# Performance work log

Measured on AMD Instinct MI355X. Metric: run time of the kernel, lower is better.

## Reference

```python
import math
import jax, jax.numpy as jnp
import numpy as np

NUM_HEADS = 16
HEAD_DIM = 64
NB_FEATURES = 256
EPS = 1e-06
DATA_NORM = HEAD_DIM ** (-0.25)


def setup_inputs() -> dict:
    key = jax.random.key(0)
    ks = jax.random.split(key, 5)
    B, N, C = 4, 4096, 1024
    x = jax.random.normal(ks[0], (B, N, C), dtype=jnp.float32)
    w_qkv = jax.random.normal(ks[1], (C, 3 * C), dtype=jnp.float32) * (C ** -0.5)
    b_qkv = jnp.zeros((3 * C,), dtype=jnp.float32)
    w_out = jax.random.normal(ks[2], (C, C), dtype=jnp.float32) * (C ** -0.5)
    b_out = jnp.zeros((C,), dtype=jnp.float32)
    proj = jax.random.normal(ks[3], (NUM_HEADS, NB_FEATURES, HEAD_DIM), dtype=jnp.float32)
    proj = proj / jnp.linalg.norm(proj, axis=-1, keepdims=True)  # F.normalize(dim=-1)
    return {"x": x, "w_qkv": w_qkv, "b_qkv": b_qkv, "w_out": w_out, "b_out": b_out,
            "proj_matrix": proj}


def _feature_map(x, proj):
    # x: [b,h,n,d], proj: [h,m,d] -> [b,h,n,m]
    x = x * DATA_NORM
    x_proj = jnp.einsum('bhnd,hmd->bhnm', x, proj)
    sq_norms = 0.5 * jnp.sum(x * x, axis=-1, keepdims=True)
    x_proj = x_proj - sq_norms
    x_proj = x_proj - jnp.max(x_proj, axis=-1, keepdims=True)
    return (jnp.exp(x_proj) + EPS) / math.sqrt(NB_FEATURES)


def reference(x, w_qkv, b_qkv, w_out, b_out, proj_matrix):
    B, N, C = x.shape
    h, d = NUM_HEADS, HEAD_DIM
    qkv = x @ w_qkv + b_qkv                     # [B,N,3C]
    q, k, v = jnp.split(qkv, 3, axis=-1)
    to_heads = lambda z: z.reshape(B, N, h, d).transpose(0, 2, 1, 3)  # [B,h,N,d]
    q, k, v = to_heads(q), to_heads(k), to_heads(v)

    q_prime = _feature_map(q, proj_matrix)      # [B,h,N,m]
    k_prime = _feature_map(k, proj_matrix)      # [B,h,N,m]

    k_sum = jnp.sum(k_prime, axis=2)                          # [B,h,m]
    kv = jnp.einsum('bhnm,bhnd->bhmd', k_prime, v)            # [B,h,m,d]
    numerator = jnp.einsum('bhnm,bhmd->bhnd', q_prime, kv)    # [B,h,N,d]
    denominator = jnp.einsum('bhnm,bhm->bhn', q_prime, k_sum) + EPS
    out = numerator / denominator[..., None]

    out = out.transpose(0, 2, 1, 3).reshape(B, N, C)
    return out @ w_out + b_out
```

## Files before the change

kernel.cpp:

```cpp
#include <hip/hip_runtime.h>
#include <hip/hip_bf16.h>
#include <stdint.h>


#define DN 0.35355339059327379f
#define EPSF 1e-6f
#define INV_SQRT_M 0.0625f

typedef __attribute__((ext_vector_type(8))) short bf16x8;
typedef __attribute__((ext_vector_type(4))) float f32x4;

static __device__ __forceinline__ short f2bf(float f) {
    __hip_bfloat16 h = __float2bfloat16(f);
    return *(short*)&h;
}
static __device__ __forceinline__ void gload16(const void* g, void* l) {
    __builtin_amdgcn_global_load_lds(
        (const __attribute__((address_space(1))) void*)g,
        (__attribute__((address_space(3))) void*)l,
        16, 0, 0);
}

__global__ __launch_bounds__(256) void conv_x(const float* __restrict__ X,
                                              short* __restrict__ Xb) {
    int i = blockIdx.x * 256 + threadIdx.x;
    float4 v = ((const float4*)X)[i];
    short4 o;
    o.x = f2bf(v.x); o.y = f2bf(v.y); o.z = f2bf(v.z); o.w = f2bf(v.w);
    ((short4*)Xb)[i] = o;
}

__global__ __launch_bounds__(256) void convt_w(const float* __restrict__ W,
                                               short* __restrict__ WT,
                                               int K, int NN) {
    __shared__ short tile[64][66];
    int t = threadIdx.x;
    int k0 = blockIdx.y * 64, n0 = blockIdx.x * 64;
    for (int i = t; i < 4096; i += 256) {
        int r = i >> 6, c = i & 63;
        tile[r][c] = f2bf(W[(size_t)(k0 + r) * NN + n0 + c]);
    }
    __syncthreads();
    for (int i = t; i < 4096; i += 256) {
        int r = i >> 6, c = i & 63;
        WT[(size_t)(n0 + r) * K + k0 + c] = tile[c][r];
    }
}

__global__ __launch_bounds__(256) void conv_proj(const float* __restrict__ proj,
                                                 short* __restrict__ pjb) {
    int e = blockIdx.x * 256 + threadIdx.x;
    int m = (e >> 6) & 255, d = e & 63;
    int base = e & ~63;
    pjb[base + (d ^ ((m & 7) << 3))] = f2bf(proj[e]);
}

__device__ __forceinline__ void gemm_core128(const short* __restrict__ A,
                                             const short* __restrict__ BT,
                                             int rowBase, int colBase,
                                             char* smem, f32x4 acc[4][4]) {
    const int K = 1024;
    int t = threadIdx.x, lane = t & 63, w = t >> 6;
    int li = lane & 15, g = lane >> 4;
    int wm = w >> 1, wn = w & 1;

    const char* aSrc[4]; const char* bSrc[4]; int aOff[4];
#pragma unroll
    for (int c = 0; c < 4; ++c) {
        int idx = c * 256 + t;
        int r = idx >> 3, s = t & 7;
        aOff[c] = idx * 16;
        aSrc[c] = (const char*)(A + (size_t)(rowBase + r) * K + ((s ^ (r & 7)) * 8));
        bSrc[c] = (const char*)(BT + (size_t)(colBase + r) * K + ((s ^ (r & 7)) * 8));
    }
#pragma unroll
    for (int m = 0; m < 4; ++m)
#pragma unroll
        for (int n = 0; n < 4; ++n) acc[m][n] = (f32x4){0.f, 0.f, 0.f, 0.f};

#pragma unroll
    for (int c = 0; c < 4; ++c) {
        gload16(aSrc[c], smem + aOff[c]);
        gload16(bSrc[c], smem + 16384 + aOff[c]);
    }

    int swz = (li & 7) << 4;

    for (int tt = 0; tt < 16; ++tt) {
        int cur = tt & 1;
        if (tt < 15) {
            char* d = smem + (cur ^ 1) * 32768;
#pragma unroll
            for (int c = 0; c < 4; ++c) {
                gload16(aSrc[c] + (size_t)(tt + 1) * 128, d + aOff[c]);
                gload16(bSrc[c] + (size_t)(tt + 1) * 128, d + 16384 + aOff[c]);
            }
            asm volatile("s_waitcnt vmcnt(8)" ::: "memory");
        } else {
            asm volatile("s_waitcnt vmcnt(0)" ::: "memory");
        }
        __builtin_amdgcn_sched_barrier(0);
        __builtin_amdgcn_s_barrier();
        __builtin_amdgcn_sched_barrier(0);
        __builtin_amdgcn_s_setprio(1);
        const char* bA = smem + cur * 32768;
        const char* bB = bA + 16384;
#pragma unroll
        for (int ks = 0; ks < 2; ++ks) {
            int kb = ks * 64 + g * 16;
            bf16x8 af[4], bv[4];
#pragma unroll
            for (int m = 0; m < 4; ++m)
                af[m] = *(const bf16x8*)(bA + (wm * 64 + m * 16 + li) * 128 + (kb ^ swz));
#pragma unroll
            for (int n = 0; n < 4; ++n)
                bv[n] = *(const bf16x8*)(bB + (wn * 64 + n * 16 + li) * 128 + (kb ^ swz));
#pragma unroll
            for (int m = 0; m < 4; ++m)
#pragma unroll
                for (int n = 0; n < 4; ++n)
                    acc[m][n] = __builtin_amdgcn_mfma_f32_16x16x32_bf16(
                        af[m], bv[n], acc[m][n], 0, 0, 0);
        }
        __builtin_amdgcn_s_setprio(0);
        __builtin_amdgcn_sched_barrier(0);
        __builtin_amdgcn_s_barrier();
        __builtin_amdgcn_sched_barrier(0);
    }
}

__global__ __launch_bounds__(256, 2) void mfma_gemm_qkv(
        const short* __restrict__ A, const short* __restrict__ BT,
        const float* __restrict__ bias,
        short* __restrict__ Qh, short* __restrict__ Kh, short* __restrict__ Vt) {
    __shared__ __align__(16) char smem[65536];
    int t = threadIdx.x, lane = t & 63, w = t >> 6;
    int li = lane & 15, g = lane >> 4, wm = w >> 1, wn = w & 1;
    int lin = blockIdx.x;
    int bx = lin % 24, by = lin / 24;
    int rowBase = by * 128, colBase = bx * 128;

    f32x4 acc[4][4];
    gemm_core128(A, BT, rowBase, colBase, smem, acc);

    float bcol[4];
#pragma unroll
    for (int n = 0; n < 4; ++n) bcol[n] = bias[colBase + wn * 64 + n * 16 + li];
    int whichB = colBase >> 10;

    if (whichB == 2) {
#pragma unroll
        for (int n = 0; n < 4; ++n) {
            int gc = colBase + wn * 64 + n * 16 + li;
            int hh = (gc & 1023) >> 6, dd = gc & 63;
#pragma unroll
            for (int m = 0; m < 4; ++m) {
                int gr0 = rowBase + wm * 64 + m * 16 + g * 4;
                int b = gr0 >> 12, nn0 = gr0 & 4095;
                short4 o;
                o.x = f2bf(acc[m][n][0] + bcol[n]);
                o.y = f2bf(acc[m][n][1] + bcol[n]);
                o.z = f2bf(acc[m][n][2] + bcol[n]);
                o.w = f2bf(acc[m][n][3] + bcol[n]);
                int nsw = (nn0 & ~63) | ((nn0 & 63) ^ ((dd & 7) << 3));
                *(short4*)&Vt[((size_t)(b * 16 + hh) * 64 + dd) * 4096 + nsw] = o;
            }
        }
    } else {
        short* dst = (whichB == 0) ? Qh : Kh;
        int hh = ((colBase + wn * 64) & 1023) >> 6;
        float* wreg = (float*)(smem + w * 8704);
#pragma unroll
        for (int r = 0; r < 2; ++r) {
#pragma unroll
            for (int mi = 0; mi < 2; ++mi)
#pragma unroll
                for (int n = 0; n < 4; ++n)
#pragma unroll
                    for (int jj = 0; jj < 4; ++jj)
                        wreg[(mi * 16 + g * 4 + jj) * 68 + n * 16 + li] =
                            (acc[2 * r + mi][n][jj] + bcol[n]) * DN;
            int row = lane >> 1, h2 = lane & 1;
            int tok = rowBase + wm * 64 + r * 32 + row;
            int b = tok >> 12, nn = tok & 4095;
            size_t base = ((size_t)(b * 16 + hh) * 4096 + nn) * 64;
#pragma unroll
            for (int k = 0; k < 4; ++k) {
                float4 v0 = *(const float4*)&wreg[row * 68 + h2 * 32 + k * 8];
                float4 v1 = *(const float4*)&wreg[row * 68 + h2 * 32 + k * 8 + 4];
                bf16x8 ov;
                ov[0] = f2bf(v0.x); ov[1] = f2bf(v0.y);
                ov[2] = f2bf(v0.z); ov[3] = f2bf(v0.w);
                ov[4] = f2bf(v1.x); ov[5] = f2bf(v1.y);
                ov[6] = f2bf(v1.z); ov[7] = f2bf(v1.w);
                int dgrp = (h2 * 4 + k) ^ (tok & 7);
                *(bf16x8*)&dst[base + dgrp * 8] = ov;
            }
        }
    }
}

__global__ __launch_bounds__(256, 2) void mfma_gemm_out(
        const short* __restrict__ A, const short* __restrict__ BT,
        const float* __restrict__ bias, float* __restrict__ C) {
    __shared__ __align__(16) char smem[65536];
    int t = threadIdx.x, lane = t & 63, w = t >> 6;
    int li = lane & 15, g = lane >> 4, wm = w >> 1, wn = w & 1;
    int lin = blockIdx.x;
    int bx = lin & 7, by = lin >> 3;
    int rowBase = by * 128, colBase = bx * 128;

    f32x4 acc[4][4];
    gemm_core128(A, BT, rowBase, colBase, smem, acc);

    float bcol[4];
#pragma unroll
    for (int n = 0; n < 4; ++n) bcol[n] = bias[colBase + wn * 64 + n * 16 + li];
    float* wreg = (float*)(smem + w * 8704);
#pragma unroll
    for (int r = 0; r < 2; ++r) {
#pragma unroll
        for (int mi = 0; mi < 2; ++mi)
#pragma unroll
            for (int n = 0; n < 4; ++n)
#pragma unroll
                for (int jj = 0; jj < 4; ++jj)
                    wreg[(mi * 16 + g * 4 + jj) * 68 + n * 16 + li] =
                        acc[2 * r + mi][n][jj] + bcol[n];
        int row = lane >> 1, h2 = lane & 1;
        int gr = rowBase + wm * 64 + r * 32 + row;
        float* cp = C + (size_t)gr * 1024 + colBase + wn * 64 + h2 * 32;
#pragma unroll
        for (int k = 0; k < 8; ++k)
            *(float4*)&cp[k * 4] = *(const float4*)&wreg[row * 68 + h2 * 32 + k * 4];
    }
}

__global__ __launch_bounds__(256) void fmap_mfma(const short* __restrict__ Kh,
                                                 const short* __restrict__ Vt,
                                                 const short* __restrict__ pjb,
                                                 float* __restrict__ kvpart,
                                                 float* __restrict__ kspart) {
    int bh = blockIdx.y, ch = blockIdx.x, h = bh & 15;
    int t = threadIdx.x, lane = t & 63, w = t >> 6;
    int g = lane >> 4, li = lane & 15;
    __shared__ __align__(16) short pj[256 * 64];
    __shared__ __align__(16) short kt[64 * 64];
    __shared__ __align__(16) short vt[64 * 64];
    __shared__ __align__(16) short Pl[4][64 * 40];
    __shared__ __align__(16) float maxw[4][64];

    const short* kbase = Kh + ((size_t)bh * 4096 + ch * 512) * 64;
    const short* vbase = Vt + (size_t)bh * 64 * 4096 + ch * 512;

    {
        const short* psrc = pjb + (size_t)h * 16384;
#pragma unroll
        for (int c2 = 0; c2 < 8; ++c2) {
            int c = 8 * w + c2;
            gload16(psrc + c * 512 + lane * 8, pj + c * 512);
        }
#pragma unroll
        for (int c2 = 0; c2 < 2; ++c2) {
            int c = 2 * w + c2;
            gload16(kbase + c * 512 + lane * 8, kt + c * 512);
            int d = 8 * c + (lane >> 3);
            gload16(vbase + (size_t)d * 4096 + (lane & 7) * 8, vt + c * 512);
        }
    }
    __syncthreads();

    f32x4 acc[4][4];
#pragma unroll
    for (int i = 0; i < 4; ++i)
#pragma unroll
        for (int j = 0; j < 4; ++j) acc[i][j] = (f32x4){0.f, 0.f, 0.f, 0.f};
    float ksacc[4] = {0.f, 0.f, 0.f, 0.f};

    int swz = (li & 7) << 4;

    for (int tile = 0; tile < 8; ++tile) {
        bf16x8 rk0, rk1, rv0, rv1;
        if (tile < 7) {
            int c0 = 2 * w, c1 = 2 * w + 1;
            size_t kof = (size_t)((tile + 1) * 64) * 64;
            rk0 = *(const bf16x8*)(kbase + kof + c0 * 512 + lane * 8);
            rk1 = *(const bf16x8*)(kbase + kof + c1 * 512 + lane * 8);
            int d0 = 8 * c0 + (lane >> 3), d1 = 8 * c1 + (lane >> 3);
            rv0 = *(const bf16x8*)(vbase + (size_t)d0 * 4096 + (tile + 1) * 64 + (lane & 7) * 8);
            rv1 = *(const bf16x8*)(vbase + (size_t)d1 * 4096 + (tile + 1) * 64 + (lane & 7) * 8);
        }

        f32x4 sacc[4][4];
#pragma unroll
        for (int i = 0; i < 4; ++i)
#pragma unroll
            for (int j = 0; j < 4; ++j) sacc[i][j] = (f32x4){0.f, 0.f, 0.f, 0.f};
#pragma unroll
        for (int ks = 0; ks < 2; ++ks) {
            int kb = ks * 64 + g * 16;
            bf16x8 afr[4], bfr[4];
#pragma unroll
            for (int ni = 0; ni < 4; ++ni)
                afr[ni] = *(const bf16x8*)((const char*)kt +
                           (16 * ni + li) * 128 + (kb ^ swz));
#pragma unroll
            for (int mi = 0; mi < 4; ++mi)
                bfr[mi] = *(const bf16x8*)((const char*)pj +
                           (64 * w + 16 * mi + li) * 128 + (kb ^ swz));
#pragma unroll
            for (int ni = 0; ni < 4; ++ni)
#pragma unroll
                for (int mi = 0; mi < 4; ++mi)
                    sacc[ni][mi] = __builtin_amdgcn_mfma_f32_16x16x32_bf16(
                        afr[ni], bfr[mi], sacc[ni][mi], 0, 0, 0);
        }

        float mxl[4][4];
#pragma unroll
        for (int ni = 0; ni < 4; ++ni)
#pragma unroll
            for (int jj = 0; jj < 4; ++jj) {
                float m0 = fmaxf(sacc[ni][0][jj], sacc[ni][1][jj]);
                float m1 = fmaxf(sacc[ni][2][jj], sacc[ni][3][jj]);
                mxl[ni][jj] = fmaxf(m0, m1);
            }
#pragma unroll
        for (int off = 1; off <= 8; off <<= 1)
#pragma unroll
            for (int ni = 0; ni < 4; ++ni)
#pragma unroll
                for (int jj = 0; jj < 4; ++jj)
                    mxl[ni][jj] = fmaxf(mxl[ni][jj], __shfl_xor(mxl[ni][jj], off));
        if (li == 0) {
#pragma unroll
            for (int ni = 0; ni < 4; ++ni)
                *(float4*)&maxw[w][16 * ni + 4 * g] =
                    make_float4(mxl[ni][0], mxl[ni][1], mxl[ni][2], mxl[ni][3]);
        }
        __syncthreads();

#pragma unroll
        for (int hf = 0; hf < 2; ++hf) {
#pragma unroll
            for (int ni2 = 0; ni2 < 2; ++ni2) {
                int ni = 2 * hf + ni2;
                float4 a0 = *(const float4*)&maxw[0][16 * ni + 4 * g];
                float4 a1 = *(const float4*)&maxw[1][16 * ni + 4 * g];
                float4 a2 = *(const float4*)&maxw[2][16 * ni + 4 * g];
                float4 a3 = *(const float4*)&maxw[3][16 * ni + 4 * g];
                float mm[4];
                mm[0] = fmaxf(fmaxf(a0.x, a1.x), fmaxf(a2.x, a3.x));
                mm[1] = fmaxf(fmaxf(a0.y, a1.y), fmaxf(a2.y, a3.y));
                mm[2] = fmaxf(fmaxf(a0.z, a1.z), fmaxf(a2.z, a3.z));
                mm[3] = fmaxf(fmaxf(a0.w, a1.w), fmaxf(a2.w, a3.w));
#pragma unroll
                for (int mi = 0; mi < 4; ++mi) {
                    float p0 = (__expf(sacc[ni][mi][0] - mm[0]) + EPSF) * INV_SQRT_M;
                    float p1 = (__expf(sacc[ni][mi][1] - mm[1]) + EPSF) * INV_SQRT_M;
                    float p2 = (__expf(sacc[ni][mi][2] - mm[2]) + EPSF) * INV_SQRT_M;
                    float p3 = (__expf(sacc[ni][mi][3] - mm[3]) + EPSF) * INV_SQRT_M;
                    ksacc[mi] += (p0 + p1) + (p2 + p3);
                    uint32_t u0 = (uint32_t)(uint16_t)f2bf(p0) |
                                  ((uint32_t)(uint16_t)f2bf(p1) << 16);
                    uint32_t u1 = (uint32_t)(uint16_t)f2bf(p2) |
                                  ((uint32_t)(uint16_t)f2bf(p3) << 16);
                    int m_l = 16 * mi + li;
                    *(uint2*)((char*)Pl[w] + m_l * 80 + 32 * ni2 + 8 * g) =
                        make_uint2(u0, u1);
                }
            }
#pragma unroll
            for (int mi = 0; mi < 4; ++mi) {
                bf16x8 pa = *(const bf16x8*)((const char*)Pl[w] +
                             (16 * mi + li) * 80 + 16 * g);
#pragma unroll
                for (int di = 0; di < 4; ++di) {
                    bf16x8 bv = *(const bf16x8*)((const char*)vt +
                                 (16 * di + li) * 128 + ((64 * hf + 16 * g) ^ swz));
                    acc[mi][di] = __builtin_amdgcn_mfma_f32_16x16x32_bf16(
                        pa, bv, acc[mi][di], 0, 0, 0);
                }
            }
        }
        __syncthreads();
        if (tile < 7) {
            int c0 = 2 * w, c1 = 2 * w + 1;
            *(bf16x8*)((char*)kt + c0 * 1024 + lane * 16) = rk0;
            *(bf16x8*)((char*)kt + c1 * 1024 + lane * 16) = rk1;
            *(bf16x8*)((char*)vt + c0 * 1024 + lane * 16) = rv0;
            *(bf16x8*)((char*)vt + c1 * 1024 + lane * 16) = rv1;
            __syncthreads();
        }
    }

#pragma unroll
    for (int mi = 0; mi < 4; ++mi) {
        ksacc[mi] += __shfl_xor(ksacc[mi], 16);
        ksacc[mi] += __shfl_xor(ksacc[mi], 32);
    }
    if (lane < 16) {
#pragma unroll
        for (int mi = 0; mi < 4; ++mi)
            kspart[(bh * 8 + ch) * 256 + 64 * w + 16 * mi + li] = ksacc[mi];
    }
    float* kvb = kvpart + (size_t)(bh * 8 + ch) * 16384;
#pragma unroll
    for (int mi = 0; mi < 4; ++mi)
#pragma unroll
        for (int di = 0; di < 4; ++di) {
            int d = 16 * di + li, m0 = 64 * w + 16 * mi + 4 * g;
            *(float4*)&kvb[d * 256 + m0] =
                make_float4(acc[mi][di][0], acc[mi][di][1],
                            acc[mi][di][2], acc[mi][di][3]);
        }
}

__global__ __launch_bounds__(256) void reduce_kv(const float* __restrict__ kvpart,
                                                 const float* __restrict__ kspart,
                                                 short* __restrict__ kvsT) {
    int bh = blockIdx.y, bx = blockIdx.x, t = threadIdx.x;
    if (bx < 4) {
#pragma unroll
        for (int i = 0; i < 16; ++i) {
            int idx = t + i * 256;
            int d = 16 * bx + (idx >> 8), m = idx & 255;
            float s = 0.f;
            size_t base = ((size_t)(bh * 8) * 64 + d) * 256 + m;
#pragma unroll
            for (int c = 0; c < 8; ++c) s += kvpart[base + (size_t)c * 16384];
            int widx = (m & 128) + ((m & 127) ^ ((d & 7) << 3));
            kvsT[((size_t)bh * 80 + d) * 256 + widx] = f2bf(s);
        }
    } else {
        float s = 0.f;
#pragma unroll
        for (int c = 0; c < 8; ++c) s += kspart[((bh * 8 + c) << 8) + t];
        kvsT[((size_t)bh * 80 + 64) * 256 + t] = f2bf(s);
        for (int i = t; i < 15 * 256; i += 256) {
            int r = 65 + (i >> 8), cc = i & 255;
            kvsT[((size_t)bh * 80 + r) * 256 + cc] = 0;
        }
    }
}

__global__ __launch_bounds__(256) void contract_mfma(
        const short* __restrict__ Qh,
        const short* __restrict__ pjb,
        const short* __restrict__ kvsT,
        short* __restrict__ attn) {
    int bh = blockIdx.y, rb = blockIdx.x, h = bh & 15, b = bh >> 4;
    int t = threadIdx.x, lane = t & 63, w = t >> 6;
    __shared__ __align__(16) short qs[128 * 64];
    __shared__ __align__(16) short pj[128 * 64];
    __shared__ __align__(16) short Pl[64 * 128];
    __shared__ __align__(16) short kvl[80 * 128];

    {
        const short* src = Qh + ((size_t)bh * 4096 + rb * 128) * 64;
#pragma unroll
        for (int c2 = 0; c2 < 4; ++c2) {
            int c = 4 * w + c2;
            gload16(src + (c * 8 + (lane >> 3)) * 64 + (lane & 7) * 8,
                    qs + c * 512);
        }
    }

    f32x4 acc5[2][5];
#pragma unroll
    for (int rg = 0; rg < 2; ++rg)
#pragma unroll
        for (int i = 0; i < 5; ++i) acc5[rg][i] = (f32x4){0.f, 0.f, 0.f, 0.f};

    int g = lane >> 4, li = lane & 15;

    for (int half = 0; half < 2; ++half) {
        const short* psrc = pjb + (size_t)h * 16384 + half * 8192;
#pragma unroll
        for (int c2 = 0; c2 < 4; ++c2) {
            int c = 4 * w + c2;
            gload16(psrc + (c * 8 + (lane >> 3)) * 64 + (lane & 7) * 8,
                    pj + c * 512);
        }
        const short* ksrc = kvsT + (size_t)bh * 80 * 256 + half * 128;
#pragma unroll
        for (int c2 = 0; c2 < 5; ++c2) {
            int c = 5 * w + c2;
            gload16(ksrc + (c * 4 + (lane >> 4)) * 256 + (lane & 15) * 8,
                    kvl + c * 512);
        }
        __syncthreads();

#pragma unroll
        for (int rg = 0; rg < 2; ++rg) {
            f32x4 sacc[2][4];
#pragma unroll
            for (int mi = 0; mi < 2; ++mi)
#pragma unroll
                for (int ni = 0; ni < 4; ++ni) sacc[mi][ni] = (f32x4){0.f, 0.f, 0.f, 0.f};
#pragma unroll
            for (int ks = 0; ks < 2; ++ks) {
                int kbyte = ks * 64 + g * 16;
                bf16x8 afr[2], bfr[4];
#pragma unroll
                for (int mi = 0; mi < 2; ++mi) {
                    int mr = 32 * w + 16 * mi + li;
                    afr[mi] = *(const bf16x8*)((const char*)pj +
                               mr * 128 + (kbyte ^ ((mr & 7) << 4)));
                }
#pragma unroll
                for (int ni = 0; ni < 4; ++ni) {
                    int qr = rg * 64 + 16 * ni + li;
                    bfr[ni] = *(const bf16x8*)((const char*)qs +
                               qr * 128 + (kbyte ^ ((qr & 7) << 4)));
                }
#pragma unroll
                for (int mi = 0; mi < 2; ++mi)
#pragma unroll
                    for (int ni = 0; ni < 4; ++ni)
                        sacc[mi][ni] = __builtin_amdgcn_mfma_f32_16x16x32_bf16(
                            afr[mi], bfr[ni], sacc[mi][ni], 0, 0, 0);
            }

#pragma unroll
            for (int mi = 0; mi < 2; ++mi) {
                int m0 = 32 * w + 16 * mi + 4 * g;
#pragma unroll
                for (int ni = 0; ni < 4; ++ni) {
                    int row = 16 * ni + li;
                    float e0 = (__expf(sacc[mi][ni][0]) + EPSF) * INV_SQRT_M;
                    float e1 = (__expf(sacc[mi][ni][1]) + EPSF) * INV_SQRT_M;
                    float e2 = (__expf(sacc[mi][ni][2]) + EPSF) * INV_SQRT_M;
                    float e3 = (__expf(sacc[mi][ni][3]) + EPSF) * INV_SQRT_M;
                    uint32_t u0 = (uint32_t)(uint16_t)f2bf(e0) |
                                  ((uint32_t)(uint16_t)f2bf(e1) << 16);
                    uint32_t u1 = (uint32_t)(uint16_t)f2bf(e2) |
                                  ((uint32_t)(uint16_t)f2bf(e3) << 16);
                    int byte = row * 256 + ((m0 * 2) ^ ((row & 7) << 4));
                    *(uint2*)((char*)Pl + byte) = make_uint2(u0, u1);
                }
            }
            __syncthreads();

            int rowA = 16 * w + li;
            int abase = rowA * 256;
            int asw = (rowA & 7) << 4;
#pragma unroll
            for (int ks = 0; ks < 4; ++ks) {
                int kbyte = ks * 64 + g * 16;
                bf16x8 pa = *(const bf16x8*)((const char*)Pl + abase + (kbyte ^ asw));
#pragma unroll
                for (int ni = 0; ni < 5; ++ni) {
                    int rowB = 16 * ni + li;
                    bf16x8 bv = *(const bf16x8*)((const char*)kvl +
                                 rowB * 256 + (kbyte ^ ((rowB & 7) << 4)));
                    acc5[rg][ni] = __builtin_amdgcn_mfma_f32_16x16x32_bf16(
                        pa, bv, acc5[rg][ni], 0, 0, 0);
                }
            }
            __syncthreads();
        }
    }

#pragma unroll
    for (int rg = 0; rg < 2; ++rg) {
        float dj[4];
#pragma unroll
        for (int jj = 0; jj < 4; ++jj)
            dj[jj] = __shfl(acc5[rg][4][jj], lane & 48) + EPSF;
#pragma unroll
        for (int ni = 0; ni < 4; ++ni) {
            int d = 16 * ni + li;
#pragma unroll
            for (int jj = 0; jj < 4; ++jj) {
                int n = rb * 128 + rg * 64 + 16 * w + 4 * g + jj;
                attn[((size_t)b * 4096 + n) * 1024 + h * 64 + d] =
                    f2bf(acc5[rg][ni][jj] / dj[jj]);
            }
        }
    }
}

extern "C" void kernel_launch(void* const* d_in, const int* in_sizes, int n_in,
                              void* d_out, int out_size, void* d_ws, size_t ws_size,
                              hipStream_t stream) {
    const float* x      = (const float*)d_in[0];
    const float* w_qkv  = (const float*)d_in[1];
    const float* b_qkv  = (const float*)d_in[2];
    const float* w_out  = (const float*)d_in[3];
    const float* b_out  = (const float*)d_in[4];
    const float* proj   = (const float*)d_in[5];
    float* out = (float*)d_out;

    char* w = (char*)d_ws;
    short* xb     = (short*)(w);
    short* wqT    = (short*)(w + 33554432);
    short* wOT    = (short*)(w + 39845888);
    short* Qh     = (short*)(w + 41943040);
    short* Kh     = (short*)(w + 75497472);
    short* Vt     = (short*)(w + 109051904);
    float* kvpart = (float*)(w);
    float* kspart = (float*)(w + 142606336);
    short* kvsT   = (short*)(w + 143130624);
    short* pjb    = (short*)(w + 145752064);
    short* attn   = Kh;

    conv_x<<<dim3(16384), 256, 0, stream>>>(x, xb);
    convt_w<<<dim3(48, 16), 256, 0, stream>>>(w_qkv, wqT, 1024, 3072);
    convt_w<<<dim3(16, 16), 256, 0, stream>>>(w_out, wOT, 1024, 1024);
    conv_proj<<<dim3(1024), 256, 0, stream>>>(proj, pjb);
    mfma_gemm_qkv<<<dim3(3072), 256, 0, stream>>>(xb, wqT, b_qkv, Qh, Kh, Vt);
    fmap_mfma<<<dim3(8, 64), 256, 0, stream>>>(Kh, Vt, pjb, kvpart, kspart);
    reduce_kv<<<dim3(5, 64), 256, 0, stream>>>(kvpart, kspart, kvsT);
    contract_mfma<<<dim3(32, 64), 256, 0, stream>>>(Qh, pjb, kvsT, attn);
    mfma_gemm_out<<<dim3(1024), 256, 0, stream>>>(attn, wOT, b_out, out);
}
```

Measured before the change: 321.7 us.

## Use 256x256 GEMM tiles with 8 waves and 4-phase quadrant pipelining

Replaces the 128x128, 4-wave GEMM core with a 256x256 tile computed by 8 waves in 512-thread blocks, using 128KB of LDS. Each K-step is split into four quadrant phases that interleave staged global-to-LDS loads with MFMA work under fine-grained vmcnt waits. The larger tile halves global/L2 traffic per FLOP for both the QKV and output projections. The cost is a single block per CU, a much more complex schedule, and fewer blocks: 256 for the output GEMM, which may underfill the GPU.

```diff
diff --git a/kernel.cpp b/kernel.cpp
--- a/kernel.cpp
+++ b/kernel.cpp
@@ -55,185 +55,241 @@
     pjb[base + (d ^ ((m & 7) << 3))] = f2bf(proj[e]);
 }
 
-__device__ __forceinline__ void gemm_core128(const short* __restrict__ A,
-                                             const short* __restrict__ BT,
-                                             int rowBase, int colBase,
-                                             char* smem, f32x4 acc[4][4]) {
+template<int Q, int S>
+static __device__ __forceinline__ void phase_compute(
+        const char* smem, int tt, int wm, int wn, int li, int g, int swz,
+        f32x4 (&acc)[2][4][2][2]) {
+    const char* bA = smem + ((tt & 1) << 16) + (Q << 14);
+    const char* bB = smem + ((tt & 1) << 16) + 32768 + (S << 14);
+    bf16x8 af[4][2], bf[2][2];
+#pragma unroll
+    for (int fr = 0; fr < 4; ++fr) {
+        int row = wm * 64 + fr * 16 + li;
+#pragma unroll
+        for (int kk = 0; kk < 2; ++kk)
+            af[fr][kk] = *(const bf16x8*)(bA + row * 128 + ((kk * 64 + g * 16) ^ swz));
+    }
+#pragma unroll
+    for (int fn = 0; fn < 2; ++fn) {
+        int row = wn * 32 + fn * 16 + li;
+#pragma unroll
+        for (int kk = 0; kk < 2; ++kk)
+            bf[fn][kk] = *(const bf16x8*)(bB + row * 128 + ((kk * 64 + g * 16) ^ swz));
+    }
+    __builtin_amdgcn_s_setprio(1);
+#pragma unroll
+    for (int kk = 0; kk < 2; ++kk)
+#pragma unroll
+        for (int fr = 0; fr < 4; ++fr)
+#pragma unroll
+            for (int fn = 0; fn < 2; ++fn)
+                acc[Q][fr][S][fn] = __builtin_amdgcn_mfma_f32_16x16x32_bf16(
+                    af[fr][kk], bf[fn][kk], acc[Q][fr][S][fn], 0, 0, 0);
+    __builtin_amdgcn_s_setprio(0);
+}
+
+static __device__ __forceinline__ void gemm_core256(const short* __restrict__ A,
+                                                    const short* __restrict__ BT,
+                                                    int rowBase, int colBase,
+                                                    char* smem,
+                                                    f32x4 (&acc)[2][4][2][2]) {
     const int K = 1024;
-    int t = threadIdx.x, lane = t & 63, w = t >> 6;
+    int t = threadIdx.x, lane = t & 63;
     int li = lane & 15, g = lane >> 4;
-    int wm = w >> 1, wn = w & 1;
-
-    const char* aSrc[4]; const char* bSrc[4]; int aOff[4];
-#pragma unroll
-    for (int c = 0; c < 4; ++c) {
-        int idx = c * 256 + t;
-        int r = idx >> 3, s = t & 7;
-        aOff[c] = idx * 16;
-        aSrc[c] = (const char*)(A + (size_t)(rowBase + r) * K + ((s ^ (r & 7)) * 8));
-        bSrc[c] = (const char*)(BT + (size_t)(colBase + r) * K + ((s ^ (r & 7)) * 8));
-    }
-#pragma unroll
-    for (int m = 0; m < 4; ++m)
-#pragma unroll
-        for (int n = 0; n < 4; ++n) acc[m][n] = (f32x4){0.f, 0.f, 0.f, 0.f};
-
-#pragma unroll
-    for (int c = 0; c < 4; ++c) {
-        gload16(aSrc[c], smem + aOff[c]);
-        gload16(bSrc[c], smem + 16384 + aOff[c]);
-    }
-
+    int w = t >> 6, wm = w >> 2, wn = w & 3;
     int swz = (li & 7) << 4;
 
-    for (int tt = 0; tt < 16; ++tt) {
-        int cur = tt & 1;
-        if (tt < 15) {
-            char* d = smem + (cur ^ 1) * 32768;
-#pragma unroll
-            for (int c = 0; c < 4; ++c) {
-                gload16(aSrc[c] + (size_t)(tt + 1) * 128, d + aOff[c]);
-                gload16(bSrc[c] + (size_t)(tt + 1) * 128, d + 16384 + aOff[c]);
-            }
-            asm volatile("s_waitcnt vmcnt(8)" ::: "memory");
-        } else {
-            asm volatile("s_waitcnt vmcnt(0)" ::: "memory");
-        }
-        __builtin_amdgcn_sched_barrier(0);
-        __builtin_amdgcn_s_barrier();
-        __builtin_amdgcn_sched_barrier(0);
-        __builtin_amdgcn_s_setprio(1);
-        const char* bA = smem + cur * 32768;
-        const char* bB = bA + 16384;
-#pragma unroll
-        for (int ks = 0; ks < 2; ++ks) {
-            int kb = ks * 64 + g * 16;
-            bf16x8 af[4], bv[4];
-#pragma unroll
-            for (int m = 0; m < 4; ++m)
-                af[m] = *(const bf16x8*)(bA + (wm * 64 + m * 16 + li) * 128 + (kb ^ swz));
-#pragma unroll
-            for (int n = 0; n < 4; ++n)
-                bv[n] = *(const bf16x8*)(bB + (wn * 64 + n * 16 + li) * 128 + (kb ^ swz));
-#pragma unroll
-            for (int m = 0; m < 4; ++m)
-#pragma unroll
-                for (int n = 0; n < 4; ++n)
-                    acc[m][n] = __builtin_amdgcn_mfma_f32_16x16x32_bf16(
-                        af[m], bv[n], acc[m][n], 0, 0, 0);
-        }
-        __builtin_amdgcn_s_setprio(0);
-        __builtin_amdgcn_sched_barrier(0);
-        __builtin_amdgcn_s_barrier();
-        __builtin_amdgcn_sched_barrier(0);
-    }
-}
-
-__global__ __launch_bounds__(256, 2) void mfma_gemm_qkv(
+    int idxA = t, idxB = 512 + t;
+    int rA = idxA >> 3, sA = idxA & 7;
+    int rB = idxB >> 3, sB = idxB & 7;
+    const char* Ab = (const char*)(A + (size_t)rowBase * K);
+    const char* Bb = (const char*)(BT + (size_t)colBase * K);
+    int srcOffA = rA * 2048 + ((sA ^ (rA & 7)) * 16);
+    int srcOffB = rB * 2048 + ((sB ^ (rB & 7)) * 16);
+    int dstOffA = idxA * 16, dstOffB = idxB * 16;
+
+#define STG(op_, half_, tile_) do {                                           \
+    char* d_ = smem + (((tile_) & 1) << 16) + ((op_) << 15) + ((half_) << 14);\
+    const char* s_ = ((op_) ? Bb : Ab) + (half_) * 262144 + (tile_) * 128;    \
+    gload16(s_ + srcOffA, d_ + dstOffA);                                      \
+    gload16(s_ + srcOffB, d_ + dstOffB);                                      \
+} while (0)
+
+#define PH(q_, s_, vm_, dost_, sop_, shalf_, stile_) do {                     \
+    if (dost_) STG(sop_, shalf_, stile_);                                     \
+    asm volatile("s_waitcnt vmcnt(" #vm_ ")" ::: "memory");                   \
+    __builtin_amdgcn_sched_barrier(0);                                        \
+    __builtin_amdgcn_s_barrier();                                             \
+    __builtin_amdgcn_sched_barrier(0);                                        \
+    phase_compute<q_, s_>(smem, tt, wm, wn, li, g, swz, acc);                 \
+} while (0)
+
+#pragma unroll
+    for (int q = 0; q < 2; ++q)
+#pragma unroll
+        for (int fr = 0; fr < 4; ++fr)
+#pragma unroll
+            for (int s = 0; s < 2; ++s)
+#pragma unroll
+                for (int fn = 0; fn < 2; ++fn)
+                    acc[q][fr][s][fn] = (f32x4){0.f, 0.f, 0.f, 0.f};
+
+    STG(1, 0, 0);
+    STG(0, 1, 0);
+    STG(0, 0, 0);
+    STG(1, 1, 0);
+    STG(1, 0, 1);
+    STG(0, 1, 1);
+
+    for (int tt = 0; tt < 14; ++tt) {
+        PH(0, 0,  8, true, 0, 0, tt + 1);
+        PH(1, 0, 12, true, 1, 1, tt + 1);
+        PH(1, 1, 10, true, 1, 0, tt + 2);
+        PH(0, 1, 12, true, 0, 1, tt + 2);
+    }
+    {
+        int tt = 14;
+        PH(0, 0,  8, true, 0, 0, 15);
+        PH(1, 0, 12, true, 1, 1, 15);
+        PH(1, 1,  8, false, 0, 0, 0);
+        PH(0, 1,  8, false, 0, 0, 0);
+    }
+    {
+        int tt = 15;
+        PH(0, 0, 2, false, 0, 0, 0);
+        PH(1, 0, 4, false, 0, 0, 0);
+        PH(1, 1, 0, false, 0, 0, 0);
+        PH(0, 1, 0, false, 0, 0, 0);
+    }
+    __builtin_amdgcn_s_barrier();
+#undef PH
+#undef STG
+}
+
+__global__ __launch_bounds__(512) void mfma_gemm_qkv(
         const short* __restrict__ A, const short* __restrict__ BT,
         const float* __restrict__ bias,
         short* __restrict__ Qh, short* __restrict__ Kh, short* __restrict__ Vt) {
-    __shared__ __align__(16) char smem[65536];
+    __shared__ __align__(16) char smem[131072];
+    int lin = blockIdx.x;
+    int bx = lin % 12, by = lin / 12;
+    int rowBase = by * 256, colBase = bx * 256;
+
+    f32x4 acc[2][4][2][2];
+    gemm_core256(A, BT, rowBase, colBase, smem, acc);
+
     int t = threadIdx.x, lane = t & 63, w = t >> 6;
-    int li = lane & 15, g = lane >> 4, wm = w >> 1, wn = w & 1;
-    int lin = blockIdx.x;
-    int bx = lin % 24, by = lin / 24;
-    int rowBase = by * 128, colBase = bx * 128;
-
-    f32x4 acc[4][4];
-    gemm_core128(A, BT, rowBase, colBase, smem, acc);
-
-    float bcol[4];
-#pragma unroll
-    for (int n = 0; n < 4; ++n) bcol[n] = bias[colBase + wn * 64 + n * 16 + li];
+    int li = lane & 15, g = lane >> 4, wm = w >> 2, wn = w & 3;
+    float bcol[2][2];
+#pragma unroll
+    for (int s = 0; s < 2; ++s)
+#pragma unroll
+        for (int fn = 0; fn < 2; ++fn)
+            bcol[s][fn] = bias[colBase + s * 128 + wn * 32 + fn * 16 + li];
     int whichB = colBase >> 10;
 
     if (whichB == 2) {
 #pragma unroll
-        for (int n = 0; n < 4; ++n) {
-            int gc = colBase + wn * 64 + n * 16 + li;
-            int hh = (gc & 1023) >> 6, dd = gc & 63;
-#pragma unroll
-            for (int m = 0; m < 4; ++m) {
-                int gr0 = rowBase + wm * 64 + m * 16 + g * 4;
-                int b = gr0 >> 12, nn0 = gr0 & 4095;
-                short4 o;
-                o.x = f2bf(acc[m][n][0] + bcol[n]);
-                o.y = f2bf(acc[m][n][1] + bcol[n]);
-                o.z = f2bf(acc[m][n][2] + bcol[n]);
-                o.w = f2bf(acc[m][n][3] + bcol[n]);
-                int nsw = (nn0 & ~63) | ((nn0 & 63) ^ ((dd & 7) << 3));
-                *(short4*)&Vt[((size_t)(b * 16 + hh) * 64 + dd) * 4096 + nsw] = o;
-            }
-        }
+        for (int s = 0; s < 2; ++s)
+#pragma unroll
+            for (int fn = 0; fn < 2; ++fn) {
+                int dd = (wn & 1) * 32 + fn * 16 + li;
+                int hh = ((colBase & 1023) >> 6) + s * 2 + (wn >> 1);
+#pragma unroll
+                for (int q = 0; q < 2; ++q)
+#pragma unroll
+                    for (int fr = 0; fr < 4; ++fr) {
+                        int gr0 = rowBase + q * 128 + wm * 64 + fr * 16 + g * 4;
+                        int b = gr0 >> 12, nn0 = gr0 & 4095;
+                        short4 o;
+                        o.x = f2bf(acc[q][fr][s][fn][0] + bcol[s][fn]);
+                        o.y = f2bf(acc[q][fr][s][fn][1] + bcol[s][fn]);
+                        o.z = f2bf(acc[q][fr][s][fn][2] + bcol[s][fn]);
+                        o.w = f2bf(acc[q][fr][s][fn][3] + bcol[s][fn]);
+                        int nsw = (nn0 & ~63) | ((nn0 & 63) ^ ((dd & 7) << 3));
+                        *(short4*)&Vt[((size_t)(b * 16 + hh) * 64 + dd) * 4096 + nsw] = o;
+                    }
+            }
     } else {
         short* dst = (whichB == 0) ? Qh : Kh;
-        int hh = ((colBase + wn * 64) & 1023) >> 6;
-        float* wreg = (float*)(smem + w * 8704);
-#pragma unroll
-        for (int r = 0; r < 2; ++r) {
-#pragma unroll
-            for (int mi = 0; mi < 2; ++mi)
-#pragma unroll
-                for (int n = 0; n < 4; ++n)
-#pragma unroll
-                    for (int jj = 0; jj < 4; ++jj)
-                        wreg[(mi * 16 + g * 4 + jj) * 68 + n * 16 + li] =
-                            (acc[2 * r + mi][n][jj] + bcol[n]) * DN;
-            int row = lane >> 1, h2 = lane & 1;
-            int tok = rowBase + wm * 64 + r * 32 + row;
-            int b = tok >> 12, nn = tok & 4095;
-            size_t base = ((size_t)(b * 16 + hh) * 4096 + nn) * 64;
-#pragma unroll
-            for (int k = 0; k < 4; ++k) {
-                float4 v0 = *(const float4*)&wreg[row * 68 + h2 * 32 + k * 8];
-                float4 v1 = *(const float4*)&wreg[row * 68 + h2 * 32 + k * 8 + 4];
-                bf16x8 ov;
-                ov[0] = f2bf(v0.x); ov[1] = f2bf(v0.y);
-                ov[2] = f2bf(v0.z); ov[3] = f2bf(v0.w);
-                ov[4] = f2bf(v1.x); ov[5] = f2bf(v1.y);
-                ov[6] = f2bf(v1.z); ov[7] = f2bf(v1.w);
-                int dgrp = (h2 * 4 + k) ^ (tok & 7);
-                *(bf16x8*)&dst[base + dgrp * 8] = ov;
-            }
-        }
-    }
-}
-
-__global__ __launch_bounds__(256, 2) void mfma_gemm_out(
+        float* wreg = (float*)(smem + w * 5120);
+#pragma unroll
+        for (int q = 0; q < 2; ++q)
+#pragma unroll
+            for (int fp = 0; fp < 2; ++fp)
+#pragma unroll
+                for (int s = 0; s < 2; ++s) {
+                    int hh = ((colBase & 1023) >> 6) + s * 2 + (wn >> 1);
+#pragma unroll
+                    for (int fr2 = 0; fr2 < 2; ++fr2)
+#pragma unroll
+                        for (int fn = 0; fn < 2; ++fn)
+#pragma unroll
+                            for (int jj = 0; jj < 4; ++jj)
+                                wreg[(fr2 * 16 + g * 4 + jj) * 40 + fn * 16 + li] =
+                                    (acc[q][fp * 2 + fr2][s][fn][jj] + bcol[s][fn]) * DN;
+                    int row2 = lane >> 1, hh2 = lane & 1;
+                    int tok = rowBase + q * 128 + wm * 64 + fp * 32 + row2;
+                    int b = tok >> 12, nn = tok & 4095;
+                    size_t base = ((size_t)(b * 16 + hh) * 4096 + nn) * 64;
+#pragma unroll
+                    for (int k = 0; k < 2; ++k) {
+                        float4 v0 = *(const float4*)&wreg[row2 * 40 + hh2 * 16 + k * 8];
+                        float4 v1 = *(const float4*)&wreg[row2 * 40 + hh2 * 16 + k * 8 + 4];
+                        bf16x8 ov;
+                        ov[0] = f2bf(v0.x); ov[1] = f2bf(v0.y);
+                        ov[2] = f2bf(v0.z); ov[3] = f2bf(v0.w);
+                        ov[4] = f2bf(v1.x); ov[5] = f2bf(v1.y);
+                        ov[6] = f2bf(v1.z); ov[7] = f2bf(v1.w);
+                        int dgrp = ((wn & 1) * 4 + hh2 * 2 + k) ^ (tok & 7);
+                        *(bf16x8*)&dst[base + dgrp * 8] = ov;
+                    }
+                }
+    }
+}
+
+__global__ __launch_bounds__(512) void mfma_gemm_out(
         const short* __restrict__ A, const short* __restrict__ BT,
         const float* __restrict__ bias, float* __restrict__ C) {
-    __shared__ __align__(16) char smem[65536];
+    __shared__ __align__(16) char smem[131072];
+    int lin = blockIdx.x;
+    int bx = lin & 3, by = lin >> 2;
+    int rowBase = by * 256, colBase = bx * 256;
+
+    f32x4 acc[2][4][2][2];
+    gemm_core256(A, BT, rowBase, colBase, smem, acc);
+
     int t = threadIdx.x, lane = t & 63, w = t >> 6;
-    int li = lane & 15, g = lane >> 4, wm = w >> 1, wn = w & 1;
-    int lin = blockIdx.x;
-    int bx = lin & 7, by = lin >> 3;
-    int rowBase = by * 128, colBase = bx * 128;
-
-    f32x4 acc[4][4];
-    gemm_core128(A, BT, rowBase, colBase, smem, acc);
-
-    float bcol[4];
-#pragma unroll
-    for (int n = 0; n < 4; ++n) bcol[n] = bias[colBase + wn * 64 + n * 16 + li];
-    float* wreg = (float*)(smem + w * 8704);
-#pragma unroll
-    for (int r = 0; r < 2; ++r) {
-#pragma unroll
-        for (int mi = 0; mi < 2; ++mi)
-#pragma unroll
-            for (int n = 0; n < 4; ++n)
-#pragma unroll
-                for (int jj = 0; jj < 4; ++jj)
-                    wreg[(mi * 16 + g * 4 + jj) * 68 + n * 16 + li] =
-                        acc[2 * r + mi][n][jj] + bcol[n];
-        int row = lane >> 1, h2 = lane & 1;
-        int gr = rowBase + wm * 64 + r * 32 + row;
-        float* cp = C + (size_t)gr * 1024 + colBase + wn * 64 + h2 * 32;
-#pragma unroll
-        for (int k = 0; k < 8; ++k)
-            *(float4*)&cp[k * 4] = *(const float4*)&wreg[row * 68 + h2 * 32 + k * 4];
-    }
+    int li = lane & 15, g = lane >> 4, wm = w >> 2, wn = w & 3;
+    float bcol[2][2];
+#pragma unroll
+    for (int s = 0; s < 2; ++s)
+#pragma unroll
+        for (int fn = 0; fn < 2; ++fn)
+            bcol[s][fn] = bias[colBase + s * 128 + wn * 32 + fn * 16 + li];
+
+    float* wreg = (float*)(smem + w * 5120);
+#pragma unroll
+    for (int q = 0; q < 2; ++q)
+#pragma unroll
+        for (int fp = 0; fp < 2; ++fp)
+#pragma unroll
+            for (int s = 0; s < 2; ++s) {
+#pragma unroll
+                for (int fr2 = 0; fr2 < 2; ++fr2)
+#pragma unroll
+                    for (int fn = 0; fn < 2; ++fn)
+#pragma unroll
+                        for (int jj = 0; jj < 4; ++jj)
+                            wreg[(fr2 * 16 + g * 4 + jj) * 40 + fn * 16 + li] =
+                                acc[q][fp * 2 + fr2][s][fn][jj] + bcol[s][fn];
+                int row2 = lane >> 1, hh2 = lane & 1;
+                int gr = rowBase + q * 128 + wm * 64 + fp * 32 + row2;
+                float* cp = C + (size_t)gr * 1024 + colBase + s * 128 + wn * 32 + hh2 * 16;
+#pragma unroll
+                for (int k = 0; k < 4; ++k)
+                    *(float4*)&cp[k * 4] = *(const float4*)&wreg[row2 * 40 + hh2 * 16 + k * 4];
+            }
 }
 
 __global__ __launch_bounds__(256) void fmap_mfma(const short* __restrict__ Kh,
@@ -609,9 +665,9 @@
     convt_w<<<dim3(48, 16), 256, 0, stream>>>(w_qkv, wqT, 1024, 3072);
     convt_w<<<dim3(16, 16), 256, 0, stream>>>(w_out, wOT, 1024, 1024);
     conv_proj<<<dim3(1024), 256, 0, stream>>>(proj, pjb);
-    mfma_gemm_qkv<<<dim3(3072), 256, 0, stream>>>(xb, wqT, b_qkv, Qh, Kh, Vt);
+    mfma_gemm_qkv<<<dim3(768), 512, 0, stream>>>(xb, wqT, b_qkv, Qh, Kh, Vt);
     fmap_mfma<<<dim3(8, 64), 256, 0, stream>>>(Kh, Vt, pjb, kvpart, kspart);
     reduce_kv<<<dim3(5, 64), 256, 0, stream>>>(kvpart, kspart, kvsT);
     contract_mfma<<<dim3(32, 64), 256, 0, stream>>>(Qh, pjb, kvsT, attn);
-    mfma_gemm_out<<<dim3(1024), 256, 0, stream>>>(attn, wOT, b_out, out);
-}
+    mfma_gemm_out<<<dim3(256), 512, 0, stream>>>(attn, wOT, b_out, out);
+}
```

Result: faster. 311.9 us (-3.0%).
